# Performance work log

Measured on AMD Instinct MI355X. Metric: run time of the kernel, lower is better.

Reference implementation:

```python
import jax, jax.numpy as jnp
import numpy as np

B_OUT, N, L, C = 8, 128, 32, 64
H, F, OUT = 128, 32, 1


def setup_inputs() -> dict:
    key = jax.random.key(0)
    ks = jax.random.split(key, 12)
    stdv = 1.0 / np.sqrt(H)
    u = lambda k, shape: jax.random.uniform(k, shape, jnp.float32, -stdv, stdv)
    return {
        "x": jax.random.normal(ks[0], (B_OUT, N, L, C), jnp.float32),
        "Q": u(ks[1], (H, C)),            # mogrify: ht @ Q -> (B, C)
        "R": u(ks[2], (C, H)),            # mogrify: xt @ R -> (B, H)
        "Wi": u(ks[3], (C + H, H)), "bi": jnp.zeros((H,), jnp.float32),
        "Wg": u(ks[4], (C + H, H)), "bg": jnp.zeros((H,), jnp.float32),
        "Wste": u(ks[5], (C + H, H)), "bste": jnp.zeros((H,), jnp.float32),
        "Wfre": u(ks[6], (C + H, F)), "bfre": jnp.zeros((F,), jnp.float32),
        "Wom": u(ks[7], (C + H, F)), "bom": jnp.zeros((F,), jnp.float32),
        "Wo": u(ks[8], (C + 2 * H, H)), "bo": jnp.zeros((H,), jnp.float32),
        "Wa": u(ks[9], (F, 1)), "ba": jnp.zeros((1,), jnp.float32),
        "Wout": u(ks[10], (H, OUT)), "bout": jnp.zeros((OUT,), jnp.float32),
    }


def reference(x, Q, R, Wi, bi, Wg, bg, Wste, bste, Wfre, bfre, Wom, bom, Wo, bo, Wa, ba, Wout, bout):
    b = x.shape[0]
    xs = x.reshape(-1, x.shape[-2], x.shape[-1])      # (B, L, C), B = b*N
    B = xs.shape[0]
    sig, tanh = jax.nn.sigmoid, jnp.tanh
    two_pi = 2.0 * jnp.pi

    h0 = jnp.zeros((B, H), jnp.float32)
    re0 = jnp.zeros((B, H, F), jnp.float32)
    im0 = jnp.zeros((B, H, F), jnp.float32)

    def step(carry, xt):
        h, re_s, im_s = carry
        # mogrify, 5 iterations (odd: update x, even: update h)
        xt = 2.0 * sig(h @ Q) * xt
        h = 2.0 * sig(xt @ R) * h
        xt = 2.0 * sig(h @ Q) * xt
        h = 2.0 * sig(xt @ R) * h
        xt = 2.0 * sig(h @ Q) * xt

        ih = jnp.concatenate([xt, h], axis=-1)        # (B, C+H)
        omega = two_pi * sig(ih @ Wom + bom)          # (B, F)
        i_t = sig(ih @ Wi + bi)                       # (B, H)
        c_hat = sig(ih @ Wg + bg)                     # (B, H)
        f_ste = sig(ih @ Wste + bste)                 # (B, H)
        f_fre = sig(ih @ Wfre + bfre)                 # (B, F)

        f_t = f_ste[:, :, None] * f_fre[:, None, :]   # (B, H, F) outer-product forget gate
        ic = (i_t * c_hat)[:, :, None]                # (B, H, 1)
        re_s = f_t * re_s + ic * jnp.cos(omega)[:, None, :]
        im_s = f_t * im_s + ic * jnp.sin(omega)[:, None, :]

        a_t = jnp.sqrt(re_s ** 2 + im_s ** 2)          # (B, H, F) amplitude
        c_t = tanh((a_t @ Wa + ba).squeeze(-1))        # (B, H)

        oh = jnp.concatenate([xt, h, c_t], axis=-1)   # (B, C+2H)
        o_t = sig(oh @ Wo + bo)
        h = o_t * tanh(c_t)
        return (h, re_s, im_s), None

    (h_last, _, _), _ = jax.lax.scan(step, (h0, re0, im0), jnp.swapaxes(xs, 0, 1))
    out = (h_last @ Wout + bout).squeeze()            # (B,) since OUT == 1
    return out.reshape(b, -1)
```

## Files before the change

### kernel.cpp

```cpp
#include <hip/hip_runtime.h>
#include <math.h>

namespace {
constexpr int LSEQ = 32;
constexpr int CDIM = 64;
constexpr int HDIM = 128;
constexpr int FDIM = 32;
constexpr float TWO_PI = 6.28318530717958647692f;

__device__ __forceinline__ float sigf(float x) { return 1.0f / (1.0f + __expf(-x)); }
__device__ __forceinline__ float tanh_fast(float x) { return 1.0f - 2.0f / (__expf(2.0f * x) + 1.0f); }
}

__global__ __launch_bounds__(512, 1)
void sfm_lstm_r9(const float* __restrict__ x,
                 const float* __restrict__ Q, const float* __restrict__ R,
                 const float* __restrict__ Wi, const float* __restrict__ bi,
                 const float* __restrict__ Wg, const float* __restrict__ bg,
                 const float* __restrict__ Wste, const float* __restrict__ bste,
                 const float* __restrict__ Wfre, const float* __restrict__ bfre,
                 const float* __restrict__ Wom, const float* __restrict__ bom,
                 const float* __restrict__ Wo, const float* __restrict__ bo,
                 const float* __restrict__ Wa, const float* __restrict__ ba,
                 const float* __restrict__ Wout, const float* __restrict__ bout,
                 float* __restrict__ out)
{
    const int t = threadIdx.x;
    const int blk = blockIdx.x;

    __shared__ float sQ[HDIM * CDIM];
    __shared__ float sR[CDIM * HDIM];
    __shared__ __align__(16) float soh[320][4];
    __shared__ __align__(16) float sit[HDIM][4];
    __shared__ __align__(16) float schat[HDIM][4];
    __shared__ __align__(16) float sfste[HDIM][4];
    __shared__ __align__(16) float sffre[FDIM][4];
    __shared__ __align__(16) float scosv[FDIM][4];
    __shared__ __align__(16) float ssinv[FDIM][4];
    __shared__ __align__(16) float spart[8192];
    __shared__ float swa[FDIM];

    #pragma unroll
    for (int i = 0; i < 16; ++i) sQ[t + 512 * i] = Q[t + 512 * i];
    #pragma unroll
    for (int i = 0; i < 16; ++i) sR[t + 512 * i] = R[t + 512 * i];
    if (t < FDIM) swa[t] = Wa[t];
    soh[64 + (t >> 2)][t & 3] = 0.0f;

    const int r7 = t & 127, sA = t >> 7;
    float re[FDIM], im[FDIM];
    #pragma unroll
    for (int f = 0; f < FDIM; ++f) { re[f] = 0.0f; im[f] = 0.0f; }

    const int gks = t / 112, gg = t - gks * 112;
    const int gcol0 = 4 * gg;
    const float* wPt = Wi; int strP = HDIM;
    if      (gcol0 < 128) { wPt = Wi   + gcol0;         strP = HDIM; }
    else if (gcol0 < 256) { wPt = Wg   + (gcol0 - 128); strP = HDIM; }
    else if (gcol0 < 384) { wPt = Wste + (gcol0 - 256); strP = HDIM; }
    else if (gcol0 < 416) { wPt = Wfre + (gcol0 - 384); strP = FDIM; }
    else                  { wPt = Wom  + (gcol0 - 416); strP = FDIM; }
    wPt += (size_t)(48 * gks) * strP;

    const float* bG = bi; int reg = -1, gcol = 0;
    if      (t < 128) { bG = bi;   gcol = t;       reg = 0; }
    else if (t < 256) { bG = bg;   gcol = t - 128; reg = 1; }
    else if (t < 384) { bG = bste; gcol = t - 256; reg = 2; }
    else if (t < 416) { bG = bfre; gcol = t - 384; reg = 3; }
    else if (t < 448) { bG = bom;  gcol = t - 416; reg = 4; }
    const float gb = (reg >= 0) ? bG[gcol] : 0.0f;

    const int oks = t >> 5, og = t & 31;
    const float* woPt = Wo + 4 * og + (size_t)(20 * oks) * HDIM;
    const float bo_r = (t < 128) ? bo[t] : 0.0f;

    const float ba0 = ba[0];
    const float* xbase = x + (size_t)blk * 4 * LSEQ * CDIM;
    const int pl = t - 448;

    if (t < 256) soh[t & 63][t >> 6] = xbase[((t >> 6) * LSEQ) * CDIM + (t & 63)];
    __syncthreads();

    for (int ts = 0; ts < LSEQ; ++ts) {
        #pragma unroll
        for (int m = 0; m < 5; ++m) {
            if ((m & 1) == 0) {
                const int c = t & 63, k0 = (t >> 6) * 16;
                float a0 = 0.f, a1 = 0.f, a2 = 0.f, a3 = 0.f;
                #pragma unroll
                for (int kk = 0; kk < 16; ++kk) {
                    const int k = k0 + kk;
                    const float qv = sQ[k * CDIM + c];
                    const float4 h4 = *(const float4*)&soh[64 + k][0];
                    a0 += qv * h4.x; a1 += qv * h4.y; a2 += qv * h4.z; a3 += qv * h4.w;
                }
                *(float4*)&spart[(t >> 6) * 256 + c * 4] = make_float4(a0, a1, a2, a3);
                __syncthreads();
                if (t < 256) {
                    float v = 0.f;
                    #pragma unroll
                    for (int i = 0; i < 8; ++i) v += spart[i * 256 + t];
                    soh[t >> 2][t & 3] = 2.0f * sigf(v) * soh[t >> 2][t & 3];
                }
                __syncthreads();
            } else {
                const int j = t & 127, k0 = (t >> 7) * 16;
                float a0 = 0.f, a1 = 0.f, a2 = 0.f, a3 = 0.f;
                #pragma unroll
                for (int kk = 0; kk < 16; ++kk) {
                    const int k = k0 + kk;
                    const float rv = sR[k * HDIM + j];
                    const float4 x4 = *(const float4*)&soh[k][0];
                    a0 += rv * x4.x; a1 += rv * x4.y; a2 += rv * x4.z; a3 += rv * x4.w;
                }
                *(float4*)&spart[(t >> 7) * 512 + j * 4] = make_float4(a0, a1, a2, a3);
                __syncthreads();
                {
                    const float v = spart[t] + spart[512 + t] + spart[1024 + t] + spart[1536 + t];
                    soh[64 + (t >> 2)][t & 3] = 2.0f * sigf(v) * soh[64 + (t >> 2)][t & 3];
                }
                __syncthreads();
            }
        }

        float xn0 = 0.f, xn1 = 0.f, xn2 = 0.f, xn3 = 0.f;
        if (t < 448) {
            float a00 = 0.f, a01 = 0.f, a02 = 0.f, a03 = 0.f;
            float a10 = 0.f, a11 = 0.f, a12 = 0.f, a13 = 0.f;
            float a20 = 0.f, a21 = 0.f, a22 = 0.f, a23 = 0.f;
            float a30 = 0.f, a31 = 0.f, a32 = 0.f, a33 = 0.f;
            const float* wp = wPt;
            const int kb = 48 * gks;
            #pragma unroll 8
            for (int kk = 0; kk < 48; ++kk) {
                const float4 w4 = *(const float4*)wp; wp += strP;
                const float4 i4 = *(const float4*)&soh[kb + kk][0];
                a00 += w4.x * i4.x; a01 += w4.x * i4.y; a02 += w4.x * i4.z; a03 += w4.x * i4.w;
                a10 += w4.y * i4.x; a11 += w4.y * i4.y; a12 += w4.y * i4.z; a13 += w4.y * i4.w;
                a20 += w4.z * i4.x; a21 += w4.z * i4.y; a22 += w4.z * i4.z; a23 += w4.z * i4.w;
                a30 += w4.w * i4.x; a31 += w4.w * i4.y; a32 += w4.w * i4.z; a33 += w4.w * i4.w;
            }
            float* sp = &spart[(gks * 448 + gcol0) * 4];
            *(float4*)(sp)      = make_float4(a00, a01, a02, a03);
            *(float4*)(sp + 4)  = make_float4(a10, a11, a12, a13);
            *(float4*)(sp + 8)  = make_float4(a20, a21, a22, a23);
            *(float4*)(sp + 12) = make_float4(a30, a31, a32, a33);
        } else if (ts + 1 < LSEQ) {
            xn0 = xbase[(0 * LSEQ + ts + 1) * CDIM + pl];
            xn1 = xbase[(1 * LSEQ + ts + 1) * CDIM + pl];
            xn2 = xbase[(2 * LSEQ + ts + 1) * CDIM + pl];
            xn3 = xbase[(3 * LSEQ + ts + 1) * CDIM + pl];
        }
        __syncthreads();

        if (reg >= 0) {
            float4 v = make_float4(0.f, 0.f, 0.f, 0.f);
            #pragma unroll
            for (int ks = 0; ks < 4; ++ks) {
                const float4 p4 = *(const float4*)&spart[(ks * 448 + t) * 4];
                v.x += p4.x; v.y += p4.y; v.z += p4.z; v.w += p4.w;
            }
            v.x += gb; v.y += gb; v.z += gb; v.w += gb;
            if (reg == 4) {
                const float o0 = TWO_PI * sigf(v.x), o1 = TWO_PI * sigf(v.y);
                const float o2 = TWO_PI * sigf(v.z), o3 = TWO_PI * sigf(v.w);
                *(float4*)&scosv[gcol][0] = make_float4(__cosf(o0), __cosf(o1), __cosf(o2), __cosf(o3));
                *(float4*)&ssinv[gcol][0] = make_float4(__sinf(o0), __sinf(o1), __sinf(o2), __sinf(o3));
            } else {
                float* d = (reg == 0) ? &sit[0][0] : (reg == 1) ? &schat[0][0]
                         : (reg == 2) ? &sfste[0][0] : &sffre[0][0];
                *(float4*)&d[gcol * 4] = make_float4(sigf(v.x), sigf(v.y), sigf(v.z), sigf(v.w));
            }
        }
        __syncthreads();

        {
            const float ic = sit[r7][sA] * schat[r7][sA];
            const float fs = sfste[r7][sA];
            float acc = 0.f;
            #pragma unroll
            for (int f = 0; f < FDIM; ++f) {
                const float ft = fs * sffre[f][sA];
                const float cv = scosv[f][sA], sv = ssinv[f][sA];
                re[f] = ft * re[f] + ic * cv;
                im[f] = ft * im[f] + ic * sv;
                acc += sqrtf(re[f] * re[f] + im[f] * im[f]) * swa[f];
            }
            soh[192 + r7][sA] = tanh_fast(acc + ba0);
        }
        __syncthreads();

        {
            float a00 = 0.f, a01 = 0.f, a02 = 0.f, a03 = 0.f;
            float a10 = 0.f, a11 = 0.f, a12 = 0.f, a13 = 0.f;
            float a20 = 0.f, a21 = 0.f, a22 = 0.f, a23 = 0.f;
            float a30 = 0.f, a31 = 0.f, a32 = 0.f, a33 = 0.f;
            const float* wp = woPt;
            const int kb = 20 * oks;
            #pragma unroll 5
            for (int kk = 0; kk < 20; ++kk) {
                const float4 w4 = *(const float4*)wp; wp += HDIM;
                const float4 i4 = *(const float4*)&soh[kb + kk][0];
                a00 += w4.x * i4.x; a01 += w4.x * i4.y; a02 += w4.x * i4.z; a03 += w4.x * i4.w;
                a10 += w4.y * i4.x; a11 += w4.y * i4.y; a12 += w4.y * i4.z; a13 += w4.y * i4.w;
                a20 += w4.z * i4.x; a21 += w4.z * i4.y; a22 += w4.z * i4.z; a23 += w4.z * i4.w;
                a30 += w4.w * i4.x; a31 += w4.w * i4.y; a32 += w4.w * i4.z; a33 += w4.w * i4.w;
            }
            float* sp = &spart[(oks * 128 + 4 * og) * 4];
            *(float4*)(sp)      = make_float4(a00, a01, a02, a03);
            *(float4*)(sp + 4)  = make_float4(a10, a11, a12, a13);
            *(float4*)(sp + 8)  = make_float4(a20, a21, a22, a23);
            *(float4*)(sp + 12) = make_float4(a30, a31, a32, a33);
        }
        __syncthreads();

        if (t < 128) {
            float4 v = make_float4(0.f, 0.f, 0.f, 0.f);
            #pragma unroll
            for (int ks = 0; ks < 16; ++ks) {
                const float4 p4 = *(const float4*)&spart[(ks * 128 + t) * 4];
                v.x += p4.x; v.y += p4.y; v.z += p4.z; v.w += p4.w;
            }
            const float4 ct4 = *(const float4*)&soh[192 + t][0];
            float4 h4;
            h4.x = sigf(v.x + bo_r) * tanh_fast(ct4.x);
            h4.y = sigf(v.y + bo_r) * tanh_fast(ct4.y);
            h4.z = sigf(v.z + bo_r) * tanh_fast(ct4.z);
            h4.w = sigf(v.w + bo_r) * tanh_fast(ct4.w);
            *(float4*)&soh[64 + t][0] = h4;
        } else if (t >= 448 && ts + 1 < LSEQ) {
            soh[pl][0] = xn0; soh[pl][1] = xn1;
            soh[pl][2] = xn2; soh[pl][3] = xn3;
        }
        __syncthreads();
    }

    if (t < 256) {
        const int w = t >> 6, l = t & 63;
        float p = soh[64 + l][w] * Wout[l] + soh[128 + l][w] * Wout[64 + l];
        #pragma unroll
        for (int off = 32; off > 0; off >>= 1) p += __shfl_xor(p, off);
        if (l == 0) out[blk * 4 + w] = p + bout[0];
    }
}

extern "C" void kernel_launch(void* const* d_in, const int* in_sizes, int n_in,
                              void* d_out, int out_size, void* d_ws, size_t ws_size,
                              hipStream_t stream) {
    const float* x    = (const float*)d_in[0];
    const float* Q    = (const float*)d_in[1];
    const float* R    = (const float*)d_in[2];
    const float* Wi   = (const float*)d_in[3];
    const float* bi   = (const float*)d_in[4];
    const float* Wg   = (const float*)d_in[5];
    const float* bg   = (const float*)d_in[6];
    const float* Wste = (const float*)d_in[7];
    const float* bste = (const float*)d_in[8];
    const float* Wfre = (const float*)d_in[9];
    const float* bfre = (const float*)d_in[10];
    const float* Wom  = (const float*)d_in[11];
    const float* bom  = (const float*)d_in[12];
    const float* Wo   = (const float*)d_in[13];
    const float* bo   = (const float*)d_in[14];
    const float* Wa   = (const float*)d_in[15];
    const float* ba   = (const float*)d_in[16];
    const float* Wout = (const float*)d_in[17];
    const float* bout = (const float*)d_in[18];
    float* out = (float*)d_out;

    sfm_lstm_r9<<<dim3(256), dim3(512), 0, stream>>>(
        x, Q, R, Wi, bi, Wg, bg, Wste, bste, Wfre, bfre, Wom, bom,
        Wo, bo, Wa, ba, Wout, bout, out);
}
```

Before: 384.6 us.

## Hold Q, R and Wo weights in registers and allow two blocks per CU

Moves the mogrify matrices Q and R out of shared memory into per-thread register arrays, and caches each thread's Wo slice as twenty float4 registers instead of reloading it from global memory every timestep. Shared memory shrinks, and the launch bound is raised to two 512-thread blocks per CU. The aim is to cut LDS and global traffic inside the recurrent loop. The cost is a much larger register footprint on top of the existing 64-float re/im state, under a tighter per-thread register cap, so spilling is likely. The grid of 256 blocks may also not gain from the higher occupancy target.

```diff
diff --git a/kernel.cpp b/kernel.cpp
--- a/kernel.cpp
+++ b/kernel.cpp
@@ -12,24 +12,22 @@
 __device__ __forceinline__ float tanh_fast(float x) { return 1.0f - 2.0f / (__expf(2.0f * x) + 1.0f); }
 }
 
-__global__ __launch_bounds__(512, 1)
-void sfm_lstm_r9(const float* __restrict__ x,
-                 const float* __restrict__ Q, const float* __restrict__ R,
-                 const float* __restrict__ Wi, const float* __restrict__ bi,
-                 const float* __restrict__ Wg, const float* __restrict__ bg,
-                 const float* __restrict__ Wste, const float* __restrict__ bste,
-                 const float* __restrict__ Wfre, const float* __restrict__ bfre,
-                 const float* __restrict__ Wom, const float* __restrict__ bom,
-                 const float* __restrict__ Wo, const float* __restrict__ bo,
-                 const float* __restrict__ Wa, const float* __restrict__ ba,
-                 const float* __restrict__ Wout, const float* __restrict__ bout,
-                 float* __restrict__ out)
+__global__ __launch_bounds__(512, 2)
+void sfm_lstm_r10(const float* __restrict__ x,
+                  const float* __restrict__ Q, const float* __restrict__ R,
+                  const float* __restrict__ Wi, const float* __restrict__ bi,
+                  const float* __restrict__ Wg, const float* __restrict__ bg,
+                  const float* __restrict__ Wste, const float* __restrict__ bste,
+                  const float* __restrict__ Wfre, const float* __restrict__ bfre,
+                  const float* __restrict__ Wom, const float* __restrict__ bom,
+                  const float* __restrict__ Wo, const float* __restrict__ bo,
+                  const float* __restrict__ Wa, const float* __restrict__ ba,
+                  const float* __restrict__ Wout, const float* __restrict__ bout,
+                  float* __restrict__ out)
 {
     const int t = threadIdx.x;
     const int blk = blockIdx.x;
 
-    __shared__ float sQ[HDIM * CDIM];
-    __shared__ float sR[CDIM * HDIM];
     __shared__ __align__(16) float soh[320][4];
     __shared__ __align__(16) float sit[HDIM][4];
     __shared__ __align__(16) float schat[HDIM][4];
@@ -40,10 +38,6 @@
     __shared__ __align__(16) float spart[8192];
     __shared__ float swa[FDIM];
 
-    #pragma unroll
-    for (int i = 0; i < 16; ++i) sQ[t + 512 * i] = Q[t + 512 * i];
-    #pragma unroll
-    for (int i = 0; i < 16; ++i) sR[t + 512 * i] = R[t + 512 * i];
     if (t < FDIM) swa[t] = Wa[t];
     soh[64 + (t >> 2)][t & 3] = 0.0f;
 
@@ -51,6 +45,21 @@
     float re[FDIM], im[FDIM];
     #pragma unroll
     for (int f = 0; f < FDIM; ++f) { re[f] = 0.0f; im[f] = 0.0f; }
+
+    const int mc = t & 63,  mksx = t >> 6;
+    const int mj = t & 127, mksh = t >> 7;
+    float qreg[16], rreg[16];
+    #pragma unroll
+    for (int kk = 0; kk < 16; ++kk) qreg[kk] = Q[(mksx * 16 + kk) * CDIM + mc];
+    #pragma unroll
+    for (int kk = 0; kk < 16; ++kk) rreg[kk] = R[(mksh * 16 + kk) * HDIM + mj];
+
+    const int oks = t >> 5, og = t & 31;
+    float4 wo4[20];
+    #pragma unroll
+    for (int kk = 0; kk < 20; ++kk)
+        wo4[kk] = *(const float4*)&Wo[(20 * oks + kk) * HDIM + 4 * og];
+    const float bo_r = (t < 128) ? bo[t] : 0.0f;
 
     const int gks = t / 112, gg = t - gks * 112;
     const int gcol0 = 4 * gg;
@@ -70,10 +79,6 @@
     else if (t < 448) { bG = bom;  gcol = t - 416; reg = 4; }
     const float gb = (reg >= 0) ? bG[gcol] : 0.0f;
 
-    const int oks = t >> 5, og = t & 31;
-    const float* woPt = Wo + 4 * og + (size_t)(20 * oks) * HDIM;
-    const float bo_r = (t < 128) ? bo[t] : 0.0f;
-
     const float ba0 = ba[0];
     const float* xbase = x + (size_t)blk * 4 * LSEQ * CDIM;
     const int pl = t - 448;
@@ -85,16 +90,15 @@
         #pragma unroll
         for (int m = 0; m < 5; ++m) {
             if ((m & 1) == 0) {
-                const int c = t & 63, k0 = (t >> 6) * 16;
+                const int k0 = mksx * 16;
                 float a0 = 0.f, a1 = 0.f, a2 = 0.f, a3 = 0.f;
                 #pragma unroll
                 for (int kk = 0; kk < 16; ++kk) {
-                    const int k = k0 + kk;
-                    const float qv = sQ[k * CDIM + c];
-                    const float4 h4 = *(const float4*)&soh[64 + k][0];
+                    const float qv = qreg[kk];
+                    const float4 h4 = *(const float4*)&soh[64 + k0 + kk][0];
                     a0 += qv * h4.x; a1 += qv * h4.y; a2 += qv * h4.z; a3 += qv * h4.w;
                 }
-                *(float4*)&spart[(t >> 6) * 256 + c * 4] = make_float4(a0, a1, a2, a3);
+                *(float4*)&spart[mksx * 256 + mc * 4] = make_float4(a0, a1, a2, a3);
                 __syncthreads();
                 if (t < 256) {
                     float v = 0.f;
@@ -104,16 +108,15 @@
                 }
                 __syncthreads();
             } else {
-                const int j = t & 127, k0 = (t >> 7) * 16;
+                const int k0 = mksh * 16;
                 float a0 = 0.f, a1 = 0.f, a2 = 0.f, a3 = 0.f;
                 #pragma unroll
                 for (int kk = 0; kk < 16; ++kk) {
-                    const int k = k0 + kk;
-                    const float rv = sR[k * HDIM + j];
-                    const float4 x4 = *(const float4*)&soh[k][0];
+                    const float rv = rreg[kk];
+                    const float4 x4 = *(const float4*)&soh[k0 + kk][0];
                     a0 += rv * x4.x; a1 += rv * x4.y; a2 += rv * x4.z; a3 += rv * x4.w;
                 }
-                *(float4*)&spart[(t >> 7) * 512 + j * 4] = make_float4(a0, a1, a2, a3);
+                *(float4*)&spart[mksh * 512 + mj * 4] = make_float4(a0, a1, a2, a3);
                 __syncthreads();
                 {
                     const float v = spart[t] + spart[512 + t] + spart[1024 + t] + spart[1536 + t];
@@ -195,11 +198,10 @@
             float a10 = 0.f, a11 = 0.f, a12 = 0.f, a13 = 0.f;
             float a20 = 0.f, a21 = 0.f, a22 = 0.f, a23 = 0.f;
             float a30 = 0.f, a31 = 0.f, a32 = 0.f, a33 = 0.f;
-            const float* wp = woPt;
             const int kb = 20 * oks;
-            #pragma unroll 5
+            #pragma unroll
             for (int kk = 0; kk < 20; ++kk) {
-                const float4 w4 = *(const float4*)wp; wp += HDIM;
+                const float4 w4 = wo4[kk];
                 const float4 i4 = *(const float4*)&soh[kb + kk][0];
                 a00 += w4.x * i4.x; a01 += w4.x * i4.y; a02 += w4.x * i4.z; a03 += w4.x * i4.w;
                 a10 += w4.y * i4.x; a11 += w4.y * i4.y; a12 += w4.y * i4.z; a13 += w4.y * i4.w;
@@ -268,7 +270,7 @@
     const float* bout = (const float*)d_in[18];
     float* out = (float*)d_out;
 
-    sfm_lstm_r9<<<dim3(256), dim3(512), 0, stream>>>(
+    sfm_lstm_r10<<<dim3(256), dim3(512), 0, stream>>>(
         x, Q, R, Wi, bi, Wg, bg, Wste, bste, Wfre, bfre, Wom, bom,
         Wo, bo, Wa, ba, Wout, bout, out);
 }
```

After: 1.229 ms. +219.7%, slower.
